# Kernel optimization log

Hardware: AMD Instinct MI355X
Metric: run time of the kernel (lower is better)

Reference implementation:

```python
import jax, jax.numpy as jnp
import numpy as np

B, T, N, H, F, E = 8, 64, 2048, 64, 64, 32768
G = 3 * H  # GRU gate dim


def setup_inputs() -> dict:
    key = jax.random.key(0)
    ks = jax.random.split(key, 12)
    s = 0.05
    return {
        "x": jax.random.normal(ks[0], (B, T, N, F), jnp.float32),
        "targets": jax.random.normal(ks[1], (B, T, N, 1), jnp.float32),
        "targets_mask": jax.random.uniform(ks[2], (B, T, N, 1)) > 0.2,
        "edge_index": jax.random.randint(ks[3], (2, E), 0, N),
        "W_msg": jax.random.normal(ks[4], (H, H), jnp.float32) * s,
        "b_msg": jnp.zeros((H,), jnp.float32),
        "W_mix": jax.random.normal(ks[5], (H, H + F), jnp.float32) * s,
        "b_mix": jnp.zeros((H,), jnp.float32),
        "W_ih": jax.random.normal(ks[6], (N, G, H), jnp.float32) * s,
        "W_hh": jax.random.normal(ks[7], (N, G, H), jnp.float32) * s,
        "b_ih": jnp.zeros((N, G), jnp.float32),
        "b_hh": jnp.zeros((N, G), jnp.float32),
        "W_read": jax.random.normal(ks[8], (1, H), jnp.float32) * s,
        "b_read": jnp.zeros((1,), jnp.float32),
    }


def reference(x, targets, targets_mask, edge_index,
              W_msg, b_msg, W_mix, b_mix,
              W_ih, W_hh, b_ih, b_hh, W_read, b_read):
    src, dst = edge_index[0], edge_index[1]

    def step(state, x_t):
        # state: [B,N,H], x_t: [B,N,F]
        m = jnp.einsum('bnh,gh->bng', state, W_msg) + b_msg           # state_to_message
        agg = jnp.zeros_like(m).at[:, dst, :].add(m[:, src, :])       # add-aggregate over directed edges
        mi = jnp.concatenate([agg, x_t], axis=-1)                     # [B,N,H+F]
        m2 = jnp.einsum('bnf,hf->bnh', mi, W_mix) + b_mix             # mix_input
        # per-node independent GRU cells (batched weights [N,3H,*])
        gi = jnp.einsum('bnh,ngh->bng', m2, W_ih) + b_ih
        gh = jnp.einsum('bnh,ngh->bng', state, W_hh) + b_hh
        i_r, i_z, i_n = jnp.split(gi, 3, axis=-1)
        h_r, h_z, h_n = jnp.split(gh, 3, axis=-1)
        r = jax.nn.sigmoid(i_r + h_r)
        z = jax.nn.sigmoid(i_z + h_z)
        n_cand = jnp.tanh(i_n + r * h_n)
        new_state = (1.0 - z) * n_cand + z * state
        out = jnp.einsum('bnh,oh->bno', new_state, W_read) + b_read   # readout -> [B,N,1]
        return new_state, out

    state0 = jnp.zeros((B, N, H), x.dtype)
    _, outs = jax.lax.scan(step, state0, jnp.swapaxes(x, 0, 1))       # outs: [T,B,N,1]
    outputs = jnp.swapaxes(outs, 0, 1)                                # [B,T,N,1]
    loss = 0.5 * (outputs - targets) ** 2
    mask = targets_mask.astype(loss.dtype)
    return jnp.sum(loss * mask) / jnp.sum(mask)                       # masked mean
```

## Files before the change

### kernel.cpp

```cpp
#include <hip/hip_runtime.h>
#include <math.h>

namespace {
constexpr int B = 8, T = 64, N = 2048, H = 64, F = 64, E = 32768, G = 192;
constexpr int BNH = B * N * H;
constexpr int NWELEM = N * G * H;
}

typedef __attribute__((ext_vector_type(8))) short bfrag;
typedef __attribute__((ext_vector_type(4))) float ffrag;

#define MFMA(a, b, c) __builtin_amdgcn_mfma_f32_16x16x32_bf16(a, b, c, 0, 0, 0)

__device__ __forceinline__ unsigned short f2bf(float f) {
  unsigned u = __float_as_uint(f);
  u += 0x7fffu + ((u >> 16) & 1u);
  return (unsigned short)(u >> 16);
}


__global__ __launch_bounds__(256) void init_kernel(
    float* __restrict__ state, float* __restrict__ mA,
    const float* __restrict__ b_msg, float* __restrict__ loss_acc,
    float* __restrict__ scal, int* __restrict__ deg)
{
  int stride = gridDim.x * blockDim.x;
  for (int i = blockIdx.x * blockDim.x + threadIdx.x; i < BNH; i += stride) {
    state[i] = 0.f;
    mA[i] = b_msg[i & (H - 1)];
    if (i < N) { loss_acc[i] = 0.f; deg[i] = 0; }
    if (i < 16) scal[i] = 0.f;
  }
}

__global__ __launch_bounds__(256) void conv_kernel(
    const float* __restrict__ Wi, const float* __restrict__ Wh,
    const float* __restrict__ Wm, const float* __restrict__ Wg,
    unsigned short* __restrict__ Wib, unsigned short* __restrict__ Whb,
    unsigned short* __restrict__ Wmb, unsigned short* __restrict__ Wgb)
{
  int stride = gridDim.x * blockDim.x;
  for (int i = blockIdx.x * blockDim.x + threadIdx.x; i < NWELEM; i += stride) {
    Wib[i] = f2bf(Wi[i]);
    Whb[i] = f2bf(Wh[i]);
    if (i < 64 * 128) Wmb[i] = f2bf(Wm[i]);
    if (i < 64 * 64) Wgb[i] = f2bf(Wg[i]);
  }
}

__global__ __launch_bounds__(256) void hist_kernel(const int* __restrict__ ei, int* __restrict__ deg) {
  int e = blockIdx.x * 256 + threadIdx.x;
  if (e < E) atomicAdd(&deg[ei[E + e]], 1);
}

__global__ __launch_bounds__(1024) void scan_kernel(const int* __restrict__ deg,
    int* __restrict__ row_ptr, int* __restrict__ cursor)
{
  __shared__ int s[N];
  int tid = threadIdx.x;
  s[tid] = deg[tid];
  s[tid + 1024] = deg[tid + 1024];
  __syncthreads();
  for (int off = 1; off < N; off <<= 1) {
    int v0 = (tid >= off) ? s[tid - off] : 0;
    int v1 = s[tid + 1024 - off];
    __syncthreads();
    s[tid] += v0;
    s[tid + 1024] += v1;
    __syncthreads();
  }
  row_ptr[tid + 1] = s[tid];
  row_ptr[tid + 1025] = s[tid + 1024];
  cursor[tid] = (tid == 0) ? 0 : s[tid - 1];
  cursor[tid + 1024] = s[tid + 1023];
  if (tid == 0) row_ptr[0] = 0;
}

__global__ __launch_bounds__(256) void fill_kernel(const int* __restrict__ ei,
    int* __restrict__ cursor, int* __restrict__ col_src)
{
  int e = blockIdx.x * 256 + threadIdx.x;
  if (e < E) {
    int d = ei[E + e];
    int slot = atomicAdd(&cursor[d], 1);
    col_src[slot] = ei[e];
  }
}

__global__ __launch_bounds__(256) void mask_kernel(const int* __restrict__ mask, float* __restrict__ scal) {
  int stride = gridDim.x * blockDim.x;
  int v = 0;
  for (int i = blockIdx.x * blockDim.x + threadIdx.x; i < B * T * N; i += stride)
    v += (mask[i] != 0);
  for (int o = 1; o < 64; o <<= 1) v += __shfl_xor(v, o, 64);
  if ((threadIdx.x & 63) == 0) atomicAdd(&scal[0], (float)v);
}


__global__ __launch_bounds__(256) void step_kernel(
    const float* __restrict__ x, const float* __restrict__ targets,
    const int* __restrict__ mask, float* __restrict__ state,
    const unsigned short* __restrict__ W_ihb, const unsigned short* __restrict__ W_hhb,
    const unsigned short* __restrict__ W_mixb, const unsigned short* __restrict__ W_msgb,
    const float* __restrict__ b_ih, const float* __restrict__ b_hh,
    const float* __restrict__ b_mix, const float* __restrict__ b_msg,
    const float* __restrict__ W_read, const float* __restrict__ b_read,
    const int* __restrict__ row_ptr, const int* __restrict__ col_src,
    const float* __restrict__ m_cur, float* __restrict__ m_nxt,
    float* __restrict__ loss_acc, int t)
{
  __shared__ float sts[B * H];
  __shared__ unsigned short aggA[B * 72];
  __shared__ unsigned short stsA[B * 72];
  __shared__ unsigned short m2A[B * 72];
  __shared__ unsigned short nsA[B * 72];
  __shared__ float gis[B * G];
  __shared__ float ghs[B * G];
  __shared__ float red[B];

  const int n = blockIdx.x;
  const int tid = threadIdx.x;
  const int w = tid >> 6, lane = tid & 63;
  const int mrow = lane & 15, quad = lane >> 4;

  {
    const int h = lane;
    const int b0 = 2 * w, b1 = 2 * w + 1;
    float s0 = state[((size_t)b0 * N + n) * H + h];
    float s1 = state[((size_t)b1 * N + n) * H + h];
    sts[b0 * H + h] = s0; sts[b1 * H + h] = s1;
    stsA[b0 * 72 + h] = f2bf(s0); stsA[b1 * 72 + h] = f2bf(s1);
    float a0 = 0.f, a1 = 0.f;
    const int e0 = row_ptr[n], e1 = row_ptr[n + 1];
    const float* mb0 = m_cur + (size_t)b0 * N * H;
    const float* mb1 = m_cur + (size_t)b1 * N * H;
    for (int e = e0; e < e1; ++e) {
      int src = col_src[e] * H;
      a0 += mb0[src + h];
      a1 += mb1[src + h];
    }
    aggA[b0 * 72 + h] = f2bf(a0); aggA[b1 * 72 + h] = f2bf(a1);
  }
  __syncthreads();

  {
    const int g0 = w * 16;
    bfrag za = (bfrag)0;
    bfrag a0 = (mrow < 8) ? *(const bfrag*)&aggA[mrow * 72 + quad * 8] : za;
    bfrag a1 = (mrow < 8) ? *(const bfrag*)&aggA[mrow * 72 + 32 + quad * 8] : za;
    bfrag a2 = za, a3 = za;
    if (mrow < 8) {
      const float* xp = x + (((size_t)mrow * T + t) * N + n) * F;
      float xv[8];
      *(float4*)&xv[0] = *(const float4*)(xp + quad * 8);
      *(float4*)&xv[4] = *(const float4*)(xp + quad * 8 + 4);
#pragma unroll
      for (int j = 0; j < 8; ++j) a2[j] = (short)f2bf(xv[j]);
      *(float4*)&xv[0] = *(const float4*)(xp + 32 + quad * 8);
      *(float4*)&xv[4] = *(const float4*)(xp + 32 + quad * 8 + 4);
#pragma unroll
      for (int j = 0; j < 8; ++j) a3[j] = (short)f2bf(xv[j]);
    }
    const unsigned short* wm = W_mixb + (g0 + mrow) * 128 + quad * 8;
    ffrag acc = {0.f, 0.f, 0.f, 0.f};
    acc = MFMA(a0, *(const bfrag*)(wm), acc);
    acc = MFMA(a1, *(const bfrag*)(wm + 32), acc);
    acc = MFMA(a2, *(const bfrag*)(wm + 64), acc);
    acc = MFMA(a3, *(const bfrag*)(wm + 96), acc);
    if (quad < 2) {
      float bm = b_mix[g0 + mrow];
#pragma unroll
      for (int r = 0; r < 4; ++r)
        m2A[(quad * 4 + r) * 72 + g0 + mrow] = f2bf(acc[r] + bm);
    }
  }
  __syncthreads();

  {
    bfrag za = (bfrag)0;
    bfrag am0 = (mrow < 8) ? *(const bfrag*)&m2A[mrow * 72 + quad * 8] : za;
    bfrag am1 = (mrow < 8) ? *(const bfrag*)&m2A[mrow * 72 + 32 + quad * 8] : za;
    bfrag as0 = (mrow < 8) ? *(const bfrag*)&stsA[mrow * 72 + quad * 8] : za;
    bfrag as1 = (mrow < 8) ? *(const bfrag*)&stsA[mrow * 72 + 32 + quad * 8] : za;
    const unsigned short* Wi = W_ihb + (size_t)n * G * H;
    const unsigned short* Wh = W_hhb + (size_t)n * G * H;
#pragma unroll
    for (int tt = 0; tt < 3; ++tt) {
      const int g0 = (w + tt * 4) * 16;
      const unsigned short* wri = Wi + (g0 + mrow) * H + quad * 8;
      const unsigned short* wrh = Wh + (g0 + mrow) * H + quad * 8;
      ffrag ai = {0.f, 0.f, 0.f, 0.f};
      ffrag ah = {0.f, 0.f, 0.f, 0.f};
      ai = MFMA(am0, *(const bfrag*)(wri), ai);
      ai = MFMA(am1, *(const bfrag*)(wri + 32), ai);
      ah = MFMA(as0, *(const bfrag*)(wrh), ah);
      ah = MFMA(as1, *(const bfrag*)(wrh + 32), ah);
      if (quad < 2) {
#pragma unroll
        for (int r = 0; r < 4; ++r) {
          gis[(quad * 4 + r) * G + g0 + mrow] = ai[r];
          ghs[(quad * 4 + r) * G + g0 + mrow] = ah[r];
        }
      }
    }
  }
  __syncthreads();

  {
    const int h = lane;
    const float bir = b_ih[n * G + h], biz = b_ih[n * G + 64 + h], bin_ = b_ih[n * G + 128 + h];
    const float bhr = b_hh[n * G + h], bhz = b_hh[n * G + 64 + h], bhn = b_hh[n * G + 128 + h];
    const float wrd = W_read[h];
    const float br = b_read[0];
#pragma unroll
    for (int bb = 0; bb < 2; ++bb) {
      const int b = 2 * w + bb;
      float ir = gis[b * G + h] + bir;
      float iz = gis[b * G + 64 + h] + biz;
      float in_ = gis[b * G + 128 + h] + bin_;
      float hr = ghs[b * G + h] + bhr;
      float hz = ghs[b * G + 64 + h] + bhz;
      float hn = ghs[b * G + 128 + h] + bhn;
      float r = 1.f / (1.f + __expf(-(ir + hr)));
      float z = 1.f / (1.f + __expf(-(iz + hz)));
      float pre = in_ + r * hn;
      float a = __expf(-2.f * fabsf(pre));
      float nc = copysignf((1.f - a) / (1.f + a), pre);
      float ns = (1.f - z) * nc + z * sts[b * H + h];
      state[((size_t)b * N + n) * H + h] = ns;
      nsA[b * 72 + h] = f2bf(ns);
      float v = ns * wrd;
#pragma unroll
      for (int o = 32; o >= 1; o >>= 1) v += __shfl_xor(v, o, 64);
      if (h == 0) {
        size_t idx = ((size_t)b * T + t) * N + n;
        float d = (v + br) - targets[idx];
        red[b] = (mask[idx] != 0) ? 0.5f * d * d : 0.f;
      }
    }
  }
  __syncthreads();

  {
    const int g0 = w * 16;
    bfrag za = (bfrag)0;
    bfrag an0 = (mrow < 8) ? *(const bfrag*)&nsA[mrow * 72 + quad * 8] : za;
    bfrag an1 = (mrow < 8) ? *(const bfrag*)&nsA[mrow * 72 + 32 + quad * 8] : za;
    const unsigned short* wg = W_msgb + (g0 + mrow) * H + quad * 8;
    ffrag acc = {0.f, 0.f, 0.f, 0.f};
    acc = MFMA(an0, *(const bfrag*)(wg), acc);
    acc = MFMA(an1, *(const bfrag*)(wg + 32), acc);
    if (quad < 2) {
      float bm = b_msg[g0 + mrow];
#pragma unroll
      for (int r = 0; r < 4; ++r)
        m_nxt[((size_t)(quad * 4 + r) * N + n) * H + g0 + mrow] = acc[r] + bm;
    }
  }
  if (tid == 0) {
    float s = red[0] + red[1] + red[2] + red[3] + red[4] + red[5] + red[6] + red[7];
    loss_acc[n] += s;
  }
}

__global__ __launch_bounds__(256) void final_kernel(const float* __restrict__ loss_acc,
    const float* __restrict__ scal, float* __restrict__ out)
{
  __shared__ float sred[4];
  float v = 0.f;
  for (int i = threadIdx.x; i < N; i += 256) v += loss_acc[i];
  for (int o = 1; o < 64; o <<= 1) v += __shfl_xor(v, o, 64);
  if ((threadIdx.x & 63) == 0) sred[threadIdx.x >> 6] = v;
  __syncthreads();
  if (threadIdx.x == 0) out[0] = (sred[0] + sred[1] + sred[2] + sred[3]) / scal[0];
}

extern "C" void kernel_launch(void* const* d_in, const int* in_sizes, int n_in,
                              void* d_out, int out_size, void* d_ws, size_t ws_size,
                              hipStream_t stream)
{
  const float* x       = (const float*)d_in[0];
  const float* targets = (const float*)d_in[1];
  const int*   mask    = (const int*)d_in[2];
  const int*   ei      = (const int*)d_in[3];
  const float* W_msg   = (const float*)d_in[4];
  const float* b_msg   = (const float*)d_in[5];
  const float* W_mix   = (const float*)d_in[6];
  const float* b_mix   = (const float*)d_in[7];
  const float* W_ih    = (const float*)d_in[8];
  const float* W_hh    = (const float*)d_in[9];
  const float* b_ih    = (const float*)d_in[10];
  const float* b_hh    = (const float*)d_in[11];
  const float* W_read  = (const float*)d_in[12];
  const float* b_read  = (const float*)d_in[13];
  float* out = (float*)d_out;

  float* state    = (float*)d_ws;
  float* mA       = state + BNH;
  float* mB       = mA + BNH;
  float* loss_acc = mB + BNH;
  float* scal     = loss_acc + N;
  int* deg        = (int*)(scal + 16);
  int* row_ptr    = deg + N;
  int* cursor     = row_ptr + (N + 16);
  int* col_src    = cursor + N;
  unsigned short* W_ihb  = (unsigned short*)(col_src + E);
  unsigned short* W_hhb  = W_ihb + NWELEM;
  unsigned short* W_mixb = W_hhb + NWELEM;
  unsigned short* W_msgb = W_mixb + 64 * 128;

  init_kernel<<<1024, 256, 0, stream>>>(state, mA, b_msg, loss_acc, scal, deg);
  conv_kernel<<<8192, 256, 0, stream>>>(W_ih, W_hh, W_mix, W_msg, W_ihb, W_hhb, W_mixb, W_msgb);
  hist_kernel<<<E / 256, 256, 0, stream>>>(ei, deg);
  scan_kernel<<<1, 1024, 0, stream>>>(deg, row_ptr, cursor);
  fill_kernel<<<E / 256, 256, 0, stream>>>(ei, cursor, col_src);
  mask_kernel<<<512, 256, 0, stream>>>(mask, scal);

  float* mcur = mA;
  float* mnxt = mB;
  for (int t = 0; t < T; ++t) {
    step_kernel<<<N, 256, 0, stream>>>(x, targets, mask, state,
                                       W_ihb, W_hhb, W_mixb, W_msgb,
                                       b_ih, b_hh, b_mix, b_msg, W_read, b_read,
                                       row_ptr, col_src, mcur, mnxt, loss_acc, t);
    float* tmp = mcur; mcur = mnxt; mnxt = tmp;
  }
  final_kernel<<<1, 256, 0, stream>>>(loss_acc, scal, out);
}
```

Measured before the change: 2.560 ms.

## Restructure GRU step kernel with node-major state, register-held weights and fused gates

Switches state and message buffers to a node-major [N][B][H] layout so each edge gather reads one contiguous block for all batches, and splits the edge loop across the four warps with a shared-memory partial-sum reduction. The W_hh and W_ih fragments are loaded into registers early so their global loads overlap the gather. The hidden-state matmul is issued before the first barrier, and the GRU gate math now runs directly on the MFMA accumulators instead of going through the gis/ghs shared buffers. This removes one barrier and a shared-memory round trip, at the cost of more registers per thread (launch bounds now request 4 blocks per SM) and a reworked loss reduction.

```diff
diff --git a/kernel.cpp b/kernel.cpp
--- a/kernel.cpp
+++ b/kernel.cpp
@@ -97,7 +97,7 @@
 }
 
 
-__global__ __launch_bounds__(256) void step_kernel(
+__global__ __launch_bounds__(256, 4) void step_kernel(
     const float* __restrict__ x, const float* __restrict__ targets,
     const int* __restrict__ mask, float* __restrict__ state,
     const unsigned short* __restrict__ W_ihb, const unsigned short* __restrict__ W_hhb,
@@ -109,133 +109,151 @@
     const float* __restrict__ m_cur, float* __restrict__ m_nxt,
     float* __restrict__ loss_acc, int t)
 {
-  __shared__ float sts[B * H];
-  __shared__ unsigned short aggA[B * 72];
-  __shared__ unsigned short stsA[B * 72];
-  __shared__ unsigned short m2A[B * 72];
-  __shared__ unsigned short nsA[B * 72];
-  __shared__ float gis[B * G];
-  __shared__ float ghs[B * G];
-  __shared__ float red[B];
+  __shared__ float partial[4][8][72];
+  __shared__ unsigned short m2A[8 * 72];
+  __shared__ unsigned short nsA[8 * 72];
+  __shared__ float redS[4][8];
 
   const int n = blockIdx.x;
   const int tid = threadIdx.x;
   const int w = tid >> 6, lane = tid & 63;
   const int mrow = lane & 15, quad = lane >> 4;
-
-  {
-    const int h = lane;
-    const int b0 = 2 * w, b1 = 2 * w + 1;
-    float s0 = state[((size_t)b0 * N + n) * H + h];
-    float s1 = state[((size_t)b1 * N + n) * H + h];
-    sts[b0 * H + h] = s0; sts[b1 * H + h] = s1;
-    stsA[b0 * 72 + h] = f2bf(s0); stsA[b1 * 72 + h] = f2bf(s1);
-    float a0 = 0.f, a1 = 0.f;
+  const bfrag za = (bfrag)0;
+
+  bfrag wh[6];
+  {
+    const unsigned short* Wh = W_hhb + (size_t)n * (G * H);
+#pragma unroll
+    for (int tt = 0; tt < 3; ++tt) {
+      const unsigned short* wrh = Wh + (((w + tt * 4) * 16 + mrow) * H) + quad * 8;
+      wh[2 * tt]     = *(const bfrag*)(wrh);
+      wh[2 * tt + 1] = *(const bfrag*)(wrh + 32);
+    }
+  }
+  bfrag as0 = za, as1 = za;
+  float4 xv0 = {0.f,0.f,0.f,0.f}, xv1 = {0.f,0.f,0.f,0.f};
+  float4 xv2 = {0.f,0.f,0.f,0.f}, xv3 = {0.f,0.f,0.f,0.f};
+  if (mrow < 8) {
+    const float* sp = state + (size_t)n * (B * H) + mrow * H;
+    float4 s0 = *(const float4*)(sp + quad * 8);
+    float4 s1 = *(const float4*)(sp + quad * 8 + 4);
+    float4 s2 = *(const float4*)(sp + 32 + quad * 8);
+    float4 s3 = *(const float4*)(sp + 32 + quad * 8 + 4);
+    as0[0]=(short)f2bf(s0.x); as0[1]=(short)f2bf(s0.y); as0[2]=(short)f2bf(s0.z); as0[3]=(short)f2bf(s0.w);
+    as0[4]=(short)f2bf(s1.x); as0[5]=(short)f2bf(s1.y); as0[6]=(short)f2bf(s1.z); as0[7]=(short)f2bf(s1.w);
+    as1[0]=(short)f2bf(s2.x); as1[1]=(short)f2bf(s2.y); as1[2]=(short)f2bf(s2.z); as1[3]=(short)f2bf(s2.w);
+    as1[4]=(short)f2bf(s3.x); as1[5]=(short)f2bf(s3.y); as1[6]=(short)f2bf(s3.z); as1[7]=(short)f2bf(s3.w);
+    const float* xp = x + (((size_t)mrow * T + t) * N + n) * F;
+    xv0 = *(const float4*)(xp + quad * 8);
+    xv1 = *(const float4*)(xp + quad * 8 + 4);
+    xv2 = *(const float4*)(xp + 32 + quad * 8);
+    xv3 = *(const float4*)(xp + 32 + quad * 8 + 4);
+  }
+  {
+    float acc[8] = {0.f,0.f,0.f,0.f,0.f,0.f,0.f,0.f};
     const int e0 = row_ptr[n], e1 = row_ptr[n + 1];
-    const float* mb0 = m_cur + (size_t)b0 * N * H;
-    const float* mb1 = m_cur + (size_t)b1 * N * H;
-    for (int e = e0; e < e1; ++e) {
-      int src = col_src[e] * H;
-      a0 += mb0[src + h];
-      a1 += mb1[src + h];
-    }
-    aggA[b0 * 72 + h] = f2bf(a0); aggA[b1 * 72 + h] = f2bf(a1);
-  }
-  __syncthreads();
-
+#pragma unroll 2
+    for (int e = e0 + w; e < e1; e += 4) {
+      const float* mp = m_cur + (size_t)col_src[e] * (B * H) + lane;
+#pragma unroll
+      for (int b = 0; b < 8; ++b) acc[b] += mp[b * H];
+    }
+#pragma unroll
+    for (int b = 0; b < 8; ++b) partial[w][b][lane] = acc[b];
+  }
+  ffrag ah0 = {0.f,0.f,0.f,0.f}, ah1 = {0.f,0.f,0.f,0.f}, ah2 = {0.f,0.f,0.f,0.f};
+  ah0 = MFMA(as0, wh[0], ah0); ah0 = MFMA(as1, wh[1], ah0);
+  ah1 = MFMA(as0, wh[2], ah1); ah1 = MFMA(as1, wh[3], ah1);
+  ah2 = MFMA(as0, wh[4], ah2); ah2 = MFMA(as1, wh[5], ah2);
+  __syncthreads();
+
+  bfrag wi[6];
+  {
+    const unsigned short* Wi = W_ihb + (size_t)n * (G * H);
+#pragma unroll
+    for (int tt = 0; tt < 3; ++tt) {
+      const unsigned short* wri = Wi + (((w + tt * 4) * 16 + mrow) * H) + quad * 8;
+      wi[2 * tt]     = *(const bfrag*)(wri);
+      wi[2 * tt + 1] = *(const bfrag*)(wri + 32);
+    }
+  }
   {
     const int g0 = w * 16;
-    bfrag za = (bfrag)0;
-    bfrag a0 = (mrow < 8) ? *(const bfrag*)&aggA[mrow * 72 + quad * 8] : za;
-    bfrag a1 = (mrow < 8) ? *(const bfrag*)&aggA[mrow * 72 + 32 + quad * 8] : za;
-    bfrag a2 = za, a3 = za;
+    bfrag a0 = za, a1 = za, a2 = za, a3 = za;
     if (mrow < 8) {
-      const float* xp = x + (((size_t)mrow * T + t) * N + n) * F;
-      float xv[8];
-      *(float4*)&xv[0] = *(const float4*)(xp + quad * 8);
-      *(float4*)&xv[4] = *(const float4*)(xp + quad * 8 + 4);
-#pragma unroll
-      for (int j = 0; j < 8; ++j) a2[j] = (short)f2bf(xv[j]);
-      *(float4*)&xv[0] = *(const float4*)(xp + 32 + quad * 8);
-      *(float4*)&xv[4] = *(const float4*)(xp + 32 + quad * 8 + 4);
-#pragma unroll
-      for (int j = 0; j < 8; ++j) a3[j] = (short)f2bf(xv[j]);
+      const float* p = &partial[0][mrow][quad * 8];
+#pragma unroll
+      for (int j = 0; j < 8; ++j) {
+        float s = p[j] + p[j + 576] + p[j + 1152] + p[j + 1728];
+        a0[j] = (short)f2bf(s);
+      }
+      const float* p2 = &partial[0][mrow][32 + quad * 8];
+#pragma unroll
+      for (int j = 0; j < 8; ++j) {
+        float s = p2[j] + p2[j + 576] + p2[j + 1152] + p2[j + 1728];
+        a1[j] = (short)f2bf(s);
+      }
+      a2[0]=(short)f2bf(xv0.x); a2[1]=(short)f2bf(xv0.y); a2[2]=(short)f2bf(xv0.z); a2[3]=(short)f2bf(xv0.w);
+      a2[4]=(short)f2bf(xv1.x); a2[5]=(short)f2bf(xv1.y); a2[6]=(short)f2bf(xv1.z); a2[7]=(short)f2bf(xv1.w);
+      a3[0]=(short)f2bf(xv2.x); a3[1]=(short)f2bf(xv2.y); a3[2]=(short)f2bf(xv2.z); a3[3]=(short)f2bf(xv2.w);
+      a3[4]=(short)f2bf(xv3.x); a3[5]=(short)f2bf(xv3.y); a3[6]=(short)f2bf(xv3.z); a3[7]=(short)f2bf(xv3.w);
     }
     const unsigned short* wm = W_mixb + (g0 + mrow) * 128 + quad * 8;
-    ffrag acc = {0.f, 0.f, 0.f, 0.f};
-    acc = MFMA(a0, *(const bfrag*)(wm), acc);
-    acc = MFMA(a1, *(const bfrag*)(wm + 32), acc);
-    acc = MFMA(a2, *(const bfrag*)(wm + 64), acc);
-    acc = MFMA(a3, *(const bfrag*)(wm + 96), acc);
+    ffrag accm = {0.f, 0.f, 0.f, 0.f};
+    accm = MFMA(a0, *(const bfrag*)(wm), accm);
+    accm = MFMA(a1, *(const bfrag*)(wm + 32), accm);
+    accm = MFMA(a2, *(const bfrag*)(wm + 64), accm);
+    accm = MFMA(a3, *(const bfrag*)(wm + 96), accm);
     if (quad < 2) {
       float bm = b_mix[g0 + mrow];
 #pragma unroll
       for (int r = 0; r < 4; ++r)
-        m2A[(quad * 4 + r) * 72 + g0 + mrow] = f2bf(acc[r] + bm);
-    }
-  }
-  __syncthreads();
-
-  {
-    bfrag za = (bfrag)0;
-    bfrag am0 = (mrow < 8) ? *(const bfrag*)&m2A[mrow * 72 + quad * 8] : za;
-    bfrag am1 = (mrow < 8) ? *(const bfrag*)&m2A[mrow * 72 + 32 + quad * 8] : za;
-    bfrag as0 = (mrow < 8) ? *(const bfrag*)&stsA[mrow * 72 + quad * 8] : za;
-    bfrag as1 = (mrow < 8) ? *(const bfrag*)&stsA[mrow * 72 + 32 + quad * 8] : za;
-    const unsigned short* Wi = W_ihb + (size_t)n * G * H;
-    const unsigned short* Wh = W_hhb + (size_t)n * G * H;
-#pragma unroll
-    for (int tt = 0; tt < 3; ++tt) {
-      const int g0 = (w + tt * 4) * 16;
-      const unsigned short* wri = Wi + (g0 + mrow) * H + quad * 8;
-      const unsigned short* wrh = Wh + (g0 + mrow) * H + quad * 8;
-      ffrag ai = {0.f, 0.f, 0.f, 0.f};
-      ffrag ah = {0.f, 0.f, 0.f, 0.f};
-      ai = MFMA(am0, *(const bfrag*)(wri), ai);
-      ai = MFMA(am1, *(const bfrag*)(wri + 32), ai);
-      ah = MFMA(as0, *(const bfrag*)(wrh), ah);
-      ah = MFMA(as1, *(const bfrag*)(wrh + 32), ah);
-      if (quad < 2) {
-#pragma unroll
-        for (int r = 0; r < 4; ++r) {
-          gis[(quad * 4 + r) * G + g0 + mrow] = ai[r];
-          ghs[(quad * 4 + r) * G + g0 + mrow] = ah[r];
-        }
-      }
-    }
-  }
-  __syncthreads();
-
-  {
-    const int h = lane;
-    const float bir = b_ih[n * G + h], biz = b_ih[n * G + 64 + h], bin_ = b_ih[n * G + 128 + h];
-    const float bhr = b_hh[n * G + h], bhz = b_hh[n * G + 64 + h], bhn = b_hh[n * G + 128 + h];
-    const float wrd = W_read[h];
-    const float br = b_read[0];
-#pragma unroll
-    for (int bb = 0; bb < 2; ++bb) {
-      const int b = 2 * w + bb;
-      float ir = gis[b * G + h] + bir;
-      float iz = gis[b * G + 64 + h] + biz;
-      float in_ = gis[b * G + 128 + h] + bin_;
-      float hr = ghs[b * G + h] + bhr;
-      float hz = ghs[b * G + 64 + h] + bhz;
-      float hn = ghs[b * G + 128 + h] + bhn;
-      float r = 1.f / (1.f + __expf(-(ir + hr)));
-      float z = 1.f / (1.f + __expf(-(iz + hz)));
-      float pre = in_ + r * hn;
-      float a = __expf(-2.f * fabsf(pre));
-      float nc = copysignf((1.f - a) / (1.f + a), pre);
-      float ns = (1.f - z) * nc + z * sts[b * H + h];
-      state[((size_t)b * N + n) * H + h] = ns;
-      nsA[b * 72 + h] = f2bf(ns);
-      float v = ns * wrd;
-#pragma unroll
-      for (int o = 32; o >= 1; o >>= 1) v += __shfl_xor(v, o, 64);
-      if (h == 0) {
-        size_t idx = ((size_t)b * T + t) * N + n;
-        float d = (v + br) - targets[idx];
-        red[b] = (mask[idx] != 0) ? 0.5f * d * d : 0.f;
+        m2A[(quad * 4 + r) * 72 + g0 + mrow] = f2bf(accm[r] + bm);
+    }
+  }
+  __syncthreads();
+
+  {
+    bfrag am0 = za, am1 = za;
+    if (mrow < 8) {
+      am0 = *(const bfrag*)&m2A[mrow * 72 + quad * 8];
+      am1 = *(const bfrag*)&m2A[mrow * 72 + 32 + quad * 8];
+    }
+    ffrag ai0 = {0.f,0.f,0.f,0.f}, ai1 = {0.f,0.f,0.f,0.f}, ai2 = {0.f,0.f,0.f,0.f};
+    ai0 = MFMA(am0, wi[0], ai0); ai0 = MFMA(am1, wi[1], ai0);
+    ai1 = MFMA(am0, wi[2], ai1); ai1 = MFMA(am1, wi[3], ai1);
+    ai2 = MFMA(am0, wi[4], ai2); ai2 = MFMA(am1, wi[5], ai2);
+    if (quad < 2) {
+      const int hcol = w * 16 + mrow;
+      const int bg = n * G + hcol;
+      const float bir = b_ih[bg], biz = b_ih[bg + 64], bin_ = b_ih[bg + 128];
+      const float bhr = b_hh[bg], bhz = b_hh[bg + 64], bhn = b_hh[bg + 128];
+      const float wrd = W_read[hcol];
+      float v[4];
+#pragma unroll
+      for (int r = 0; r < 4; ++r) {
+        const int b = quad * 4 + r;
+        float ir = ai0[r] + bir, iz = ai1[r] + biz, in_ = ai2[r] + bin_;
+        float hr = ah0[r] + bhr, hz = ah1[r] + bhz, hn = ah2[r] + bhn;
+        float rg = 1.f / (1.f + __expf(-(ir + hr)));
+        float z  = 1.f / (1.f + __expf(-(iz + hz)));
+        float pre = in_ + rg * hn;
+        float a = __expf(-2.f * fabsf(pre));
+        float nc = copysignf((1.f - a) / (1.f + a), pre);
+        float sold = state[(size_t)n * (B * H) + b * H + hcol];
+        float ns = (1.f - z) * nc + z * sold;
+        state[(size_t)n * (B * H) + b * H + hcol] = ns;
+        nsA[b * 72 + hcol] = f2bf(ns);
+        v[r] = ns * wrd;
+      }
+#pragma unroll
+      for (int o = 1; o < 16; o <<= 1) {
+#pragma unroll
+        for (int r = 0; r < 4; ++r) v[r] += __shfl_xor(v[r], o, 64);
+      }
+      if (mrow == 0) {
+#pragma unroll
+        for (int r = 0; r < 4; ++r) redS[w][quad * 4 + r] = v[r];
       }
     }
   }
@@ -243,23 +261,31 @@
 
   {
     const int g0 = w * 16;
-    bfrag za = (bfrag)0;
-    bfrag an0 = (mrow < 8) ? *(const bfrag*)&nsA[mrow * 72 + quad * 8] : za;
-    bfrag an1 = (mrow < 8) ? *(const bfrag*)&nsA[mrow * 72 + 32 + quad * 8] : za;
+    bfrag an0 = za, an1 = za;
+    if (mrow < 8) {
+      an0 = *(const bfrag*)&nsA[mrow * 72 + quad * 8];
+      an1 = *(const bfrag*)&nsA[mrow * 72 + 32 + quad * 8];
+    }
     const unsigned short* wg = W_msgb + (g0 + mrow) * H + quad * 8;
-    ffrag acc = {0.f, 0.f, 0.f, 0.f};
-    acc = MFMA(an0, *(const bfrag*)(wg), acc);
-    acc = MFMA(an1, *(const bfrag*)(wg + 32), acc);
+    ffrag accg = {0.f, 0.f, 0.f, 0.f};
+    accg = MFMA(an0, *(const bfrag*)(wg), accg);
+    accg = MFMA(an1, *(const bfrag*)(wg + 32), accg);
     if (quad < 2) {
       float bm = b_msg[g0 + mrow];
 #pragma unroll
       for (int r = 0; r < 4; ++r)
-        m_nxt[((size_t)(quad * 4 + r) * N + n) * H + g0 + mrow] = acc[r] + bm;
-    }
-  }
-  if (tid == 0) {
-    float s = red[0] + red[1] + red[2] + red[3] + red[4] + red[5] + red[6] + red[7];
-    loss_acc[n] += s;
+        m_nxt[(size_t)n * (B * H) + (quad * 4 + r) * H + g0 + mrow] = accg[r] + bm;
+    }
+  }
+  if (tid < 8) {
+    float vv = redS[0][tid] + redS[1][tid] + redS[2][tid] + redS[3][tid] + b_read[0];
+    size_t idx = ((size_t)tid * T + t) * N + n;
+    float d = vv - targets[idx];
+    float l = (mask[idx] != 0) ? 0.5f * d * d : 0.f;
+    l += __shfl_xor(l, 1, 64);
+    l += __shfl_xor(l, 2, 64);
+    l += __shfl_xor(l, 4, 64);
+    if (tid == 0) loss_acc[n] += l;
   }
 }
 
```

Result: slower. 2.618 ms (+2.3%).
